# Performance work log

Measured on AMD Instinct MI355X. Metric: run time of the kernel, lower is better.

The kernel has to match this reference:

```python
import jax, jax.numpy as jnp
import numpy as np

SH_C0 = 0.28209479177387814
SH_C1 = 0.4886025119029199


def quat_to_rot(q):
    # q: [..., 4] in (w, x, y, z) order, as in 3DGS
    q = q / jnp.linalg.norm(q, axis=-1, keepdims=True)
    w, x, y, z = q[..., 0], q[..., 1], q[..., 2], q[..., 3]
    R = jnp.stack([
        1 - 2 * (y * y + z * z), 2 * (x * y - w * z), 2 * (x * z + w * y),
        2 * (x * y + w * z), 1 - 2 * (x * x + z * z), 2 * (y * z - w * x),
        2 * (x * z - w * y), 2 * (y * z + w * x), 1 - 2 * (x * x + y * y)],
        axis=-1)
    return R.reshape(q.shape[:-1] + (3, 3))


def _render_one_view(xyz, feats, cov3d, opacity, c2w, intr, H, W):
    # xyz [N,3], feats [N,4,3], cov3d [N,3,3], opacity [N], c2w [4,4], intr [4]
    w2c = jnp.linalg.inv(c2w)
    Rcw, tcw = w2c[:3, :3], w2c[:3, 3]
    p = xyz @ Rcw.T + tcw                     # camera-space means [N,3]
    x, y, z = p[:, 0], p[:, 1], p[:, 2]
    valid = z > 0.2                           # near-plane cull
    zs = jnp.maximum(z, 0.2)
    fx, fy, cx, cy = intr[0], intr[1], intr[2], intr[3]
    u = fx * x / zs + cx                      # pixel-space 2D means
    v = fy * y / zs + cy
    # EWA projection Jacobian [N,2,3]
    zero = jnp.zeros_like(zs)
    J = jnp.stack([fx / zs, zero, -fx * x / (zs * zs),
                   zero, fy / zs, -fy * y / (zs * zs)], axis=-1).reshape(-1, 2, 3)
    cov_cam = jnp.einsum('ij,njk,lk->nil', Rcw, cov3d, Rcw)
    cov2d = jnp.einsum('nij,njk,nlk->nil', J, cov_cam, J)
    a = cov2d[:, 0, 0] + 0.3                  # low-pass dilation as in 3DGS
    b = cov2d[:, 0, 1]
    c = cov2d[:, 1, 1] + 0.3
    det = jnp.maximum(a * c - b * b, 1e-6)
    ca, cb, cc = c / det, -b / det, a / det   # conic (inverse 2x2 cov)
    # SH degree-1 color from view direction
    campos = c2w[:3, 3]
    d = xyz - campos
    d = d / jnp.linalg.norm(d, axis=-1, keepdims=True)
    color = (SH_C0 * feats[:, 0]
             - SH_C1 * d[:, 1:2] * feats[:, 1]
             + SH_C1 * d[:, 2:3] * feats[:, 2]
             - SH_C1 * d[:, 0:1] * feats[:, 3]) + 0.5
    color = jnp.maximum(color, 0.0)
    op = jnp.where(valid, opacity, 0.0)
    # global front-to-back depth sort (reference for the tiled sort)
    order = jnp.argsort(jnp.where(valid, z, jnp.inf))
    u, v = u[order], v[order]
    ca, cb, cc = ca[order], cb[order], cc[order]
    color, op = color[order], op[order]
    # pixel centers
    px = jnp.arange(W, dtype=xyz.dtype) + 0.5
    py = jnp.arange(H, dtype=xyz.dtype) + 0.5
    gx, gy = jnp.meshgrid(px, py)             # [H,W], gx varies along W
    dx = gx.reshape(-1, 1) - u[None, :]       # [P,N]
    dy = gy.reshape(-1, 1) - v[None, :]
    power = -0.5 * (ca * dx * dx + cc * dy * dy) - cb * dx * dy
    alpha = jnp.where(power > 0, 0.0,
                      jnp.minimum(0.99, op * jnp.exp(jnp.minimum(power, 0.0))))
    alpha = jnp.where(alpha < 1.0 / 255.0, 0.0, alpha)
    T = jnp.cumprod(1.0 - alpha, axis=-1)
    T_prev = jnp.concatenate([jnp.ones_like(T[:, :1]), T[:, :-1]], axis=-1)
    wgt = alpha * T_prev                      # [P,N] composite weights
    img = wgt @ color                         # [P,3]
    return img.reshape(H, W, 3).transpose(2, 0, 1)


def setup_inputs() -> dict:
    key = jax.random.key(0)
    ks = jax.random.split(key, 5)
    b, n, H, W = 1, 1024, 128, 128
    xyz = jax.random.normal(ks[0], (b, n, 3), dtype=jnp.float32)
    features = jax.random.normal(ks[1], (b, n, 4, 3), dtype=jnp.float32) * 0.5
    scaling = 0.01 + 0.06 * jax.random.uniform(ks[2], (b, n, 3), dtype=jnp.float32)
    rotation = jax.random.normal(ks[3], (b, n, 4), dtype=jnp.float32)
    opacity = jax.random.uniform(ks[4], (b, n, 1), dtype=jnp.float32)
    # two OpenCV cameras at radius 3 looking at the origin
    def make_c2w(angle):
        ca, sa = np.cos(angle), np.sin(angle)
        Ry = np.array([[ca, 0, sa], [0, 1, 0], [-sa, 0, ca]], dtype=np.float32)
        M = np.eye(4, dtype=np.float32)
        M[:3, :3] = Ry
        M[:3, 3] = Ry @ np.array([0.0, 0.0, -3.0], dtype=np.float32)
        return M
    C2W = jnp.asarray(np.stack([make_c2w(0.0), make_c2w(0.4)])[None])  # [1,2,4,4]
    intr = np.array([float(W), float(W), W / 2.0, H / 2.0], dtype=np.float32)
    fxfycxcy = jnp.asarray(np.broadcast_to(intr, (b, 2, 4)).copy())
    return {"xyz": xyz, "features": features, "scaling": scaling,
            "rotation": rotation, "opacity": opacity,
            "height": H, "width": W, "C2W": C2W, "fxfycxcy": fxfycxcy}


def reference(xyz, features, scaling, rotation, opacity, height, width, C2W, fxfycxcy):
    H, W = int(height), int(width)
    R = quat_to_rot(rotation)                  # [b,N,3,3]
    M = R * scaling[..., None, :]
    cov3d = M @ jnp.swapaxes(M, -1, -2)        # [b,N,3,3]
    op = opacity[..., 0]
    def per_batch(xyz_b, f_b, cov_b, op_b, c2w_b, intr_b):
        return jax.vmap(lambda c2w, intr: _render_one_view(
            xyz_b, f_b, cov_b, op_b, c2w, intr, H, W))(c2w_b, intr_b)
    return jax.vmap(per_batch)(xyz, features, cov3d, op, C2W, fxfycxcy)  # [b,v,3,H,W]
```

## Files before the change

kernel.cpp:

```cpp
#include <hip/hip_runtime.h>
#include <math.h>

#define NG 1024
#define HH 128
#define WW 128
#define NV 2
#define SH_C0 0.28209479177387814f
#define SH_C1 0.4886025119029199f

#define RECF 12

#define TILE 16
#define TPX  (WW/TILE)
#define TPY  (HH/TILE)
#define NT   (TPX*TPY)
#define RCH  256


__global__ __launch_bounds__(256) void prep_rank_kernel(
    const float* __restrict__ xyz, const float* __restrict__ feats,
    const float* __restrict__ scaling, const float* __restrict__ rotation,
    const float* __restrict__ opacity, const float* __restrict__ C2W,
    const float* __restrict__ intr, float* __restrict__ ws)
{
    __shared__ unsigned long long s_key[NG];
    __shared__ int s_cnt[256];

    const int iv  = blockIdx.x >> 3;
    const int seg = blockIdx.x & 7;
    const int t   = threadIdx.x;

    const float* c2w = C2W + iv * 16;
    const float r20 = c2w[2], r21 = c2w[6], r22 = c2w[10];
    const float tc2 = -(r20*c2w[3] + r21*c2w[7] + r22*c2w[11]);

    #pragma unroll
    for (int k = 0; k < 4; ++k) {
        const int g = k*256 + t;
        const float X = xyz[g*3+0], Y = xyz[g*3+1], Z = xyz[g*3+2];
        const float pz = r20*X + r21*Y + r22*Z + tc2;
        const float zk = (pz > 0.2f) ? pz : 100000.0f;
        s_key[g] = (((unsigned long long)__float_as_uint(zk)) << 10)
                 | (unsigned long long)(unsigned)g;
    }
    __syncthreads();

    const int g    = seg*128 + (t & 127);
    const int half = t >> 7;
    const unsigned long long ki = s_key[g];
    {
        const unsigned long long* kp = s_key + half*512;
        int cnt = 0;
        #pragma unroll 8
        for (int j = 0; j < 512; ++j)
            cnt += (kp[j] < ki) ? 1 : 0;
        s_cnt[t] = cnt;
    }
    __syncthreads();

    if (t >= 128) return;
    const int rank = s_cnt[t] + s_cnt[t+128];

    const float fx = intr[iv*4+0], fy = intr[iv*4+1];
    const float cx = intr[iv*4+2], cy = intr[iv*4+3];

    float Rcw[3][3], tcw[3];
    #pragma unroll
    for (int r = 0; r < 3; ++r)
        #pragma unroll
        for (int c = 0; c < 3; ++c)
            Rcw[r][c] = c2w[c*4 + r];
    #pragma unroll
    for (int r = 0; r < 3; ++r)
        tcw[r] = -(Rcw[r][0]*c2w[3] + Rcw[r][1]*c2w[7] + Rcw[r][2]*c2w[11]);
    const float camx = c2w[3], camy = c2w[7], camz = c2w[11];

    const float X = xyz[g*3+0], Y = xyz[g*3+1], Z = xyz[g*3+2];

    float qw = rotation[g*4+0], qx = rotation[g*4+1];
    float qy = rotation[g*4+2], qz = rotation[g*4+3];
    const float qn = rsqrtf(qw*qw + qx*qx + qy*qy + qz*qz);
    qw *= qn; qx *= qn; qy *= qn; qz *= qn;
    const float R00 = 1.f - 2.f*(qy*qy + qz*qz);
    const float R01 = 2.f*(qx*qy - qw*qz);
    const float R02 = 2.f*(qx*qz + qw*qy);
    const float R10 = 2.f*(qx*qy + qw*qz);
    const float R11 = 1.f - 2.f*(qx*qx + qz*qz);
    const float R12 = 2.f*(qy*qz - qw*qx);
    const float R20 = 2.f*(qx*qz - qw*qy);
    const float R21 = 2.f*(qy*qz + qw*qx);
    const float R22 = 1.f - 2.f*(qx*qx + qy*qy);

    const float s0 = scaling[g*3+0], s1 = scaling[g*3+1], s2 = scaling[g*3+2];
    const float M00 = R00*s0, M01 = R01*s1, M02 = R02*s2;
    const float M10 = R10*s0, M11 = R11*s1, M12 = R12*s2;
    const float M20 = R20*s0, M21 = R21*s1, M22 = R22*s2;

    const float S00 = M00*M00 + M01*M01 + M02*M02;
    const float S01 = M00*M10 + M01*M11 + M02*M12;
    const float S02 = M00*M20 + M01*M21 + M02*M22;
    const float S11 = M10*M10 + M11*M11 + M12*M12;
    const float S12 = M10*M20 + M11*M21 + M12*M22;
    const float S22 = M20*M20 + M21*M21 + M22*M22;

    float tmp[3][3];
    const float S[3][3] = {{S00,S01,S02},{S01,S11,S12},{S02,S12,S22}};
    #pragma unroll
    for (int r = 0; r < 3; ++r)
        #pragma unroll
        for (int c = 0; c < 3; ++c)
            tmp[r][c] = Rcw[r][0]*S[0][c] + Rcw[r][1]*S[1][c] + Rcw[r][2]*S[2][c];
    float C[3][3];
    #pragma unroll
    for (int r = 0; r < 3; ++r)
        #pragma unroll
        for (int c = 0; c < 3; ++c)
            C[r][c] = tmp[r][0]*Rcw[c][0] + tmp[r][1]*Rcw[c][1] + tmp[r][2]*Rcw[c][2];

    const float px_ = Rcw[0][0]*X + Rcw[0][1]*Y + Rcw[0][2]*Z + tcw[0];
    const float py_ = Rcw[1][0]*X + Rcw[1][1]*Y + Rcw[1][2]*Z + tcw[1];
    const float zf  = __uint_as_float((unsigned)(ki >> 10));
    const bool valid = zf < 99999.0f;

    const float zs = fmaxf(zf, 0.2f);
    const float izs = 1.f / zs;

    const float u = fx*px_*izs + cx;
    const float v = fy*py_*izs + cy;

    const float a00 = fx*izs;
    const float a02 = -fx*px_*izs*izs;
    const float a11 = fy*izs;
    const float a12 = -fy*py_*izs*izs;

    const float c00 = a00*a00*C[0][0] + 2.f*a00*a02*C[0][2] + a02*a02*C[2][2] + 0.3f;
    const float c01 = a00*a11*C[0][1] + a00*a12*C[0][2] + a02*a11*C[1][2] + a02*a12*C[2][2];
    const float c11 = a11*a11*C[1][1] + 2.f*a11*a12*C[1][2] + a12*a12*C[2][2] + 0.3f;

    const float det = fmaxf(c00*c11 - c01*c01, 1e-6f);
    const float idet = 1.f / det;

    float dx = X - camx, dy = Y - camy, dz = Z - camz;
    const float dn = rsqrtf(dx*dx + dy*dy + dz*dz);
    dx *= dn; dy *= dn; dz *= dn;
    const float* f = feats + g*12;
    float col[3];
    #pragma unroll
    for (int c = 0; c < 3; ++c) {
        float cc_ = SH_C0*f[0*3+c] - SH_C1*dy*f[1*3+c] + SH_C1*dz*f[2*3+c]
                    - SH_C1*dx*f[3*3+c] + 0.5f;
        col[c] = fmaxf(cc_, 0.f);
    }

    const float op = valid ? opacity[g] : 0.f;
    const float pwmin = -logf(255.f * op);

    const float Aq = -0.5f * (c11*idet);
    const float Bq = c01*idet;
    const float Cq = -0.5f * (c00*idet);

    float dumax = -1.f, dvmax = -1.f;
    if (op >= (1.f/255.f)) {
        const float L = -pwmin;
        dumax = sqrtf(2.f*L*c00);
        dvmax = sqrtf(2.f*L*c11);
    }

    float4* dst = (float4*)(ws + (size_t)(iv*NG + rank)*RECF);
    dst[0] = make_float4(u,  v,  dumax, dvmax);
    dst[1] = make_float4(Aq, Bq, Cq,    pwmin);
    dst[2] = make_float4(op, col[0], col[1], col[2]);
}

__global__ __launch_bounds__(256) void render_kernel(
    const float* __restrict__ ws, float* __restrict__ out)
{
    __shared__ unsigned short s_ids[NG];
    __shared__ int s_wsum[4];
    __shared__ float4 s_rec[RCH*3];

    const int iv   = blockIdx.x / NT;
    const int tile = blockIdx.x % NT;
    const int tx0  = (tile % TPX) * TILE;
    const int ty0  = (tile / TPX) * TILE;
    const int t    = threadIdx.x;
    const int lane = t & 63;
    const int wid  = t >> 6;

    const float xlo = tx0 + 0.5f, xhi = tx0 + TILE - 0.5f;
    const float ylo = ty0 + 0.5f, yhi = ty0 + TILE - 0.5f;

    const float4* recs = (const float4*)ws + (size_t)iv*NG*3;

    int flags = 0, cnt = 0;
    #pragma unroll
    for (int k = 0; k < 4; ++k) {
        const int gidx = t*4 + k;
        const float4 g0 = recs[gidx*3+0];
        const bool hit = (g0.z >= 0.f)
                      && (g0.x - g0.z <= xhi) && (g0.x + g0.z >= xlo)
                      && (g0.y - g0.w <= yhi) && (g0.y + g0.w >= ylo);
        flags |= (hit ? 1 : 0) << k;
        cnt   += hit ? 1 : 0;
    }

    int v = cnt;
    #pragma unroll
    for (int d = 1; d < 64; d <<= 1) {
        const int n = __shfl_up(v, d, 64);
        if (lane >= d) v += n;
    }
    if (lane == 63) s_wsum[wid] = v;
    __syncthreads();
    int waveOff = 0;
    #pragma unroll
    for (int w = 0; w < 4; ++w)
        if (w < wid) waveOff += s_wsum[w];
    const int m = s_wsum[0] + s_wsum[1] + s_wsum[2] + s_wsum[3];
    int base = waveOff + v - cnt;
    #pragma unroll
    for (int k = 0; k < 4; ++k) {
        if (flags & (1 << k)) s_ids[base++] = (unsigned short)(t*4 + k);
    }
    __syncthreads();

    const int px = tx0 + (t & (TILE-1));
    const int py = ty0 + (t >> 4);
    const float gx = px + 0.5f;
    const float gy = py + 0.5f;

    float T = 1.f, ar = 0.f, ag = 0.f, ab = 0.f;

    for (int c0 = 0; c0 < m; c0 += RCH) {
        const int nc = min(RCH, m - c0);
        for (int idx = t; idx < nc*3; idx += 256) {
            const int rid = s_ids[c0 + idx/3];
            s_rec[idx] = recs[rid*3 + idx%3];
        }
        __syncthreads();

        if (T >= 1e-5f) {
            for (int j = 0; j < nc; ++j) {
                const float4 g0 = s_rec[j*3+0];
                const float4 g1 = s_rec[j*3+1];
                const float du = gx - g0.x;
                const float dv = gy - g0.y;
                const float pw = fmaf(g1.x, du*du, fmaf(g1.z, dv*dv, g1.y*(du*dv)));
                if (pw <= 0.f && pw >= g1.w) {
                    const float4 g2 = s_rec[j*3+2];
                    const float al = fminf(0.99f, g2.x * __expf(pw));
                    if (al >= (1.f/255.f)) {
                        const float w = al * T;
                        ar += w * g2.y;
                        ag += w * g2.z;
                        ab += w * g2.w;
                        T *= (1.f - al);
                        if (T < 1e-5f) break;
                    }
                }
            }
        }
        __syncthreads();
    }

    out[((iv*3 + 0)*HH + py)*WW + px] = ar;
    out[((iv*3 + 1)*HH + py)*WW + px] = ag;
    out[((iv*3 + 2)*HH + py)*WW + px] = ab;
}

extern "C" void kernel_launch(void* const* d_in, const int* in_sizes, int n_in,
                              void* d_out, int out_size, void* d_ws, size_t ws_size,
                              hipStream_t stream) {
    const float* xyz      = (const float*)d_in[0];
    const float* feats    = (const float*)d_in[1];
    const float* scaling  = (const float*)d_in[2];
    const float* rotation = (const float*)d_in[3];
    const float* opacity  = (const float*)d_in[4];
    const float* C2W      = (const float*)d_in[7];
    const float* intr     = (const float*)d_in[8];

    float* ws  = (float*)d_ws;
    float* out = (float*)d_out;

    prep_rank_kernel<<<NV*8, 256, 0, stream>>>(
        xyz, feats, scaling, rotation, opacity, C2W, intr, ws);

    render_kernel<<<NV*NT, 256, 0, stream>>>(ws, out);
}
```

Before: 89.81 us.

## Split tile gaussian list across waves with 8x8 tiles and merge partial composites

Render tiles shrink from 16x16 to 8x8, so each of the 256 threads' four waves covers the same 64 pixels. Each wave composites a contiguous quarter of the depth-sorted gaussian list, and the four partial (color, transmittance) results are merged front-to-back through shared memory. All of a tile's records are now staged once into a larger shared buffer instead of in chunks. The prep kernel also switches xyz, rotation and feature loads to float4 vector loads. This gives four times more blocks and shorter serial loops per thread. In exchange it uses more shared memory, which may lower occupancy, and the later waves lose early termination because they cannot see earlier waves' transmittance.

Result: faster. 82.39 us (-8.3%).

```diff
diff --git a/kernel.cpp b/kernel.cpp
--- a/kernel.cpp
+++ b/kernel.cpp
@@ -10,11 +10,10 @@
 
 #define RECF 12
 
-#define TILE 16
+#define TILE 8
 #define TPX  (WW/TILE)
 #define TPY  (HH/TILE)
 #define NT   (TPX*TPY)
-#define RCH  256
 
 
 __global__ __launch_bounds__(256) void prep_rank_kernel(
@@ -34,14 +33,22 @@
     const float r20 = c2w[2], r21 = c2w[6], r22 = c2w[10];
     const float tc2 = -(r20*c2w[3] + r21*c2w[7] + r22*c2w[11]);
 
-    #pragma unroll
-    for (int k = 0; k < 4; ++k) {
-        const int g = k*256 + t;
-        const float X = xyz[g*3+0], Y = xyz[g*3+1], Z = xyz[g*3+2];
-        const float pz = r20*X + r21*Y + r22*Z + tc2;
-        const float zk = (pz > 0.2f) ? pz : 100000.0f;
-        s_key[g] = (((unsigned long long)__float_as_uint(zk)) << 10)
-                 | (unsigned long long)(unsigned)g;
+    {
+        const float4* xyz4 = (const float4*)xyz;
+        const float4 a0 = xyz4[t*3+0];
+        const float4 a1 = xyz4[t*3+1];
+        const float4 a2 = xyz4[t*3+2];
+        const float xs[4] = {a0.x, a0.w, a1.z, a2.y};
+        const float ys[4] = {a0.y, a1.x, a1.w, a2.z};
+        const float zw[4] = {a0.z, a1.y, a2.x, a2.w};
+        #pragma unroll
+        for (int k = 0; k < 4; ++k) {
+            const int g = t*4 + k;
+            const float pz = r20*xs[k] + r21*ys[k] + r22*zw[k] + tc2;
+            const float zk = (pz > 0.2f) ? pz : 100000.0f;
+            s_key[g] = (((unsigned long long)__float_as_uint(zk)) << 10)
+                     | (unsigned long long)(unsigned)g;
+        }
     }
     __syncthreads();
 
@@ -77,8 +84,8 @@
 
     const float X = xyz[g*3+0], Y = xyz[g*3+1], Z = xyz[g*3+2];
 
-    float qw = rotation[g*4+0], qx = rotation[g*4+1];
-    float qy = rotation[g*4+2], qz = rotation[g*4+3];
+    const float4 qv = ((const float4*)rotation)[g];
+    float qw = qv.x, qx = qv.y, qy = qv.z, qz = qv.w;
     const float qn = rsqrtf(qw*qw + qx*qx + qy*qy + qz*qz);
     qw *= qn; qx *= qn; qy *= qn; qz *= qn;
     const float R00 = 1.f - 2.f*(qy*qy + qz*qz);
@@ -143,14 +150,12 @@
     float dx = X - camx, dy = Y - camy, dz = Z - camz;
     const float dn = rsqrtf(dx*dx + dy*dy + dz*dz);
     dx *= dn; dy *= dn; dz *= dn;
-    const float* f = feats + g*12;
+    const float4* f4 = (const float4*)feats + g*3;
+    const float4 f0 = f4[0], f1 = f4[1], f2 = f4[2];
     float col[3];
-    #pragma unroll
-    for (int c = 0; c < 3; ++c) {
-        float cc_ = SH_C0*f[0*3+c] - SH_C1*dy*f[1*3+c] + SH_C1*dz*f[2*3+c]
-                    - SH_C1*dx*f[3*3+c] + 0.5f;
-        col[c] = fmaxf(cc_, 0.f);
-    }
+    col[0] = fmaxf(SH_C0*f0.x - SH_C1*dy*f0.w + SH_C1*dz*f1.z - SH_C1*dx*f2.y + 0.5f, 0.f);
+    col[1] = fmaxf(SH_C0*f0.y - SH_C1*dy*f1.x + SH_C1*dz*f1.w - SH_C1*dx*f2.z + 0.5f, 0.f);
+    col[2] = fmaxf(SH_C0*f0.z - SH_C1*dy*f1.y + SH_C1*dz*f2.x - SH_C1*dx*f2.w + 0.5f, 0.f);
 
     const float op = valid ? opacity[g] : 0.f;
     const float pwmin = -logf(255.f * op);
@@ -177,7 +182,8 @@
 {
     __shared__ unsigned short s_ids[NG];
     __shared__ int s_wsum[4];
-    __shared__ float4 s_rec[RCH*3];
+    __shared__ float4 s_rec[NG*3];
+    __shared__ float4 s_part[4][64];
 
     const int iv   = blockIdx.x / NT;
     const int tile = blockIdx.x % NT;
@@ -224,48 +230,61 @@
     }
     __syncthreads();
 
-    const int px = tx0 + (t & (TILE-1));
-    const int py = ty0 + (t >> 4);
-    const float gx = px + 0.5f;
-    const float gy = py + 0.5f;
+    for (int idx = t; idx < m*3; idx += 256) {
+        const int rid = s_ids[idx/3];
+        s_rec[idx] = recs[rid*3 + idx%3];
+    }
+    __syncthreads();
+
+    const float gx = tx0 + (lane & (TILE-1)) + 0.5f;
+    const float gy = ty0 + (lane >> 3) + 0.5f;
+
+    const int q  = (m + 3) >> 2;
+    const int j0 = wid * q;
+    const int j1 = min(j0 + q, m);
 
     float T = 1.f, ar = 0.f, ag = 0.f, ab = 0.f;
-
-    for (int c0 = 0; c0 < m; c0 += RCH) {
-        const int nc = min(RCH, m - c0);
-        for (int idx = t; idx < nc*3; idx += 256) {
-            const int rid = s_ids[c0 + idx/3];
-            s_rec[idx] = recs[rid*3 + idx%3];
-        }
-        __syncthreads();
-
-        if (T >= 1e-5f) {
-            for (int j = 0; j < nc; ++j) {
-                const float4 g0 = s_rec[j*3+0];
-                const float4 g1 = s_rec[j*3+1];
-                const float du = gx - g0.x;
-                const float dv = gy - g0.y;
-                const float pw = fmaf(g1.x, du*du, fmaf(g1.z, dv*dv, g1.y*(du*dv)));
-                if (pw <= 0.f && pw >= g1.w) {
-                    const float4 g2 = s_rec[j*3+2];
-                    const float al = fminf(0.99f, g2.x * __expf(pw));
-                    if (al >= (1.f/255.f)) {
-                        const float w = al * T;
-                        ar += w * g2.y;
-                        ag += w * g2.z;
-                        ab += w * g2.w;
-                        T *= (1.f - al);
-                        if (T < 1e-5f) break;
-                    }
-                }
+    for (int j = j0; j < j1; ++j) {
+        const float4 g0 = s_rec[j*3+0];
+        const float4 g1 = s_rec[j*3+1];
+        const float du = gx - g0.x;
+        const float dv = gy - g0.y;
+        const float pw = fmaf(g1.x, du*du, fmaf(g1.z, dv*dv, g1.y*(du*dv)));
+        if (pw <= 0.f && pw >= g1.w) {
+            const float4 g2 = s_rec[j*3+2];
+            const float al = fminf(0.99f, g2.x * __expf(pw));
+            if (al >= (1.f/255.f)) {
+                const float w = al * T;
+                ar += w * g2.y;
+                ag += w * g2.z;
+                ab += w * g2.w;
+                T *= (1.f - al);
+                if (T < 1e-5f) break;
             }
         }
-        __syncthreads();
-    }
-
-    out[((iv*3 + 0)*HH + py)*WW + px] = ar;
-    out[((iv*3 + 1)*HH + py)*WW + px] = ag;
-    out[((iv*3 + 2)*HH + py)*WW + px] = ab;
+    }
+    s_part[wid][lane] = make_float4(ar, ag, ab, T);
+    __syncthreads();
+
+    if (t < 64) {
+        const float4 p0 = s_part[0][t];
+        const float4 p1 = s_part[1][t];
+        const float4 p2 = s_part[2][t];
+        const float4 p3 = s_part[3][t];
+        float Ta = p0.w;
+        float r = p0.x + Ta*p1.x;
+        float g = p0.y + Ta*p1.y;
+        float b = p0.z + Ta*p1.z;
+        Ta *= p1.w;
+        r += Ta*p2.x; g += Ta*p2.y; b += Ta*p2.z;
+        Ta *= p2.w;
+        r += Ta*p3.x; g += Ta*p3.y; b += Ta*p3.z;
+        const int px = tx0 + (t & (TILE-1));
+        const int py = ty0 + (t >> 3);
+        out[((iv*3 + 0)*HH + py)*WW + px] = r;
+        out[((iv*3 + 1)*HH + py)*WW + px] = g;
+        out[((iv*3 + 2)*HH + py)*WW + px] = b;
+    }
 }
 
 extern "C" void kernel_launch(void* const* d_in, const int* in_sizes, int n_in,
```
